# Kernel optimization log

Hardware: AMD Instinct MI355X
Metric: run time of the kernel (lower is better)

The kernel has to match this reference:

```python
import jax, jax.numpy as jnp
import numpy as np

EMBED_DIM = 768
NUM_HEADS = 12
NUM_BOND_TYPES = 4
NEG_INF = -1e9


def setup_inputs() -> dict:
    key = jax.random.key(0)
    ks = jax.random.split(key, 8)
    B, N, E = 32, 512, EMBED_DIM
    x = jax.random.normal(ks[0], (B, N, E), dtype=jnp.float32)
    adj = jax.random.randint(ks[1], (B, N, N), 0, 2, dtype=jnp.int32)
    bond = jax.random.randint(ks[2], (B, N, N), 0, NUM_BOND_TYPES + 1, dtype=jnp.int32)
    # nn.Linear(E, 3E): weight (3E, E), bias (3E)
    lim_qkv = 1.0 / np.sqrt(E)
    qkv_w = jax.random.uniform(ks[3], (3 * E, E), minval=-lim_qkv, maxval=lim_qkv, dtype=jnp.float32)
    qkv_b = jax.random.uniform(ks[4], (3 * E,), minval=-lim_qkv, maxval=lim_qkv, dtype=jnp.float32)
    out_w = jax.random.uniform(ks[5], (E, E), minval=-lim_qkv, maxval=lim_qkv, dtype=jnp.float32)
    out_b = jax.random.uniform(ks[6], (E,), minval=-lim_qkv, maxval=lim_qkv, dtype=jnp.float32)
    # nn.Embedding(num_bond_types+1, 1), padding_idx=0 -> row 0 is zero
    bond_table = jax.random.normal(ks[7], (NUM_BOND_TYPES + 1, 1), dtype=jnp.float32)
    bond_table = bond_table.at[0].set(0.0)
    return {"x": x, "adj": adj, "bond": bond, "num_heads": NUM_HEADS,
            "qkv_w": qkv_w, "qkv_b": qkv_b, "out_w": out_w, "out_b": out_b,
            "bond_table": bond_table}


def reference(x, adj, bond, num_heads, qkv_w, qkv_b, out_w, out_b, bond_table):
    B, N, E = x.shape
    hd = E // num_heads
    scale = hd ** -0.5
    # enforce padding_idx=0 semantics
    bond_table = bond_table.at[0].set(0.0)
    qkv = x @ qkv_w.T + qkv_b                      # (B, N, 3E)
    qkv = qkv.reshape(B, N, 3, num_heads, hd).transpose(2, 0, 3, 1, 4)
    q, k, v = qkv[0], qkv[1], qkv[2]               # (B, h, N, hd)
    attn = jnp.einsum('bhnd,bhmd->bhnm', q, k) * scale
    attn = attn + adj.astype(x.dtype)[:, None, :, :]
    bond_bias = bond_table[bond, 0]                # (B, N, N) embedding gather
    attn = attn + bond_bias[:, None, :, :]
    attn = jnp.where(attn == 0, NEG_INF, attn)     # masked_fill(attn == 0)
    attn = jax.nn.softmax(attn, axis=-1)
    out = jnp.einsum('bhnm,bhmd->bhnd', attn, v)   # (B, h, N, hd)
    out = out.transpose(0, 2, 1, 3).reshape(B, N, E)
    return out @ out_w.T + out_b
```

## Files before the change

kernel.cpp:

```cpp
#include <hip/hip_runtime.h>
#include <hip/hip_bf16.h>

typedef __attribute__((ext_vector_type(8))) short short8;
typedef __attribute__((ext_vector_type(4))) float f32x4;
typedef __attribute__((ext_vector_type(4))) unsigned int uint4v;
typedef __attribute__((ext_vector_type(4))) int int4v;

#define MFMA16(a,b,c) __builtin_amdgcn_mfma_f32_16x16x32_bf16((a),(b),(c),0,0,0)

#define GLOAD_LDS16(g, l) \
    __builtin_amdgcn_global_load_lds((const __attribute__((address_space(1))) void*)(g), \
                                     (__attribute__((address_space(3))) void*)(l), 16, 0, 0)

__device__ __forceinline__ unsigned short f2bf(float f){
    union { float f; unsigned int u; } c; c.f = f;
    unsigned int u = c.u;
    u = (u + 0x7fffu + ((u >> 16) & 1u)) >> 16;
    return (unsigned short)u;
}
__device__ __forceinline__ float bf2f(unsigned short s){
    union { unsigned int u; float f; } c; c.u = ((unsigned int)s) << 16;
    return c.f;
}

__device__ __forceinline__ void tsplit(float f, unsigned short &h, unsigned short &l){
    unsigned int u = __builtin_bit_cast(unsigned int, f);
    float hi = __builtin_bit_cast(float, u & 0xffff0000u);
    h = (unsigned short)(u >> 16);
    l = (unsigned short)(__builtin_bit_cast(unsigned int, f - hi) >> 16);
}

__device__ __forceinline__ unsigned int pack_split(float f){
    unsigned int u = __builtin_bit_cast(unsigned int, f);
    float hi = __builtin_bit_cast(float, u & 0xffff0000u);
    unsigned int rem = __builtin_bit_cast(unsigned int, f - hi);
    return __builtin_amdgcn_perm(rem, u, 0x07060302u);
}

__device__ __forceinline__ void unpack8(uint4v u0, uint4v u1, short8& hi, short8& lo){
    uint4v h, l;
    h[0] = __builtin_amdgcn_perm(u0[1], u0[0], 0x05040100u);
    h[1] = __builtin_amdgcn_perm(u0[3], u0[2], 0x05040100u);
    h[2] = __builtin_amdgcn_perm(u1[1], u1[0], 0x05040100u);
    h[3] = __builtin_amdgcn_perm(u1[3], u1[2], 0x05040100u);
    l[0] = __builtin_amdgcn_perm(u0[1], u0[0], 0x07060302u);
    l[1] = __builtin_amdgcn_perm(u0[3], u0[2], 0x07060302u);
    l[2] = __builtin_amdgcn_perm(u1[1], u1[0], 0x07060302u);
    l[3] = __builtin_amdgcn_perm(u1[3], u1[2], 0x07060302u);
    hi = __builtin_bit_cast(short8, h);
    lo = __builtin_bit_cast(short8, l);
}


__global__ void pack_x_kernel(const float* __restrict__ x, unsigned int* __restrict__ img){
    int tid = blockIdx.x * 256 + threadIdx.x;
    int m = tid / 96, grp = tid - m * 96;
    const float* src = x + (size_t)m * 768 + grp * 8;
    f32x4 v0 = ((const f32x4*)src)[0];
    f32x4 v1 = ((const f32x4*)src)[1];
    short8 h8, l8;
    #pragma unroll
    for (int j = 0; j < 4; ++j){
        unsigned short hh, ll;
        tsplit(v0[j], hh, ll); h8[j]   = (short)hh; l8[j]   = (short)ll;
        tsplit(v1[j], hh, ll); h8[4+j] = (short)hh; l8[4+j] = (short)ll;
    }
    int mt = m >> 7, row = m & 127, kt = grp >> 2, gi = grp & 3;
    int sw = (row & 7) << 4;
    char* bp = (char*)img + ((size_t)(mt*24 + kt))*16384 + row*128;
    *(short8*)(bp + ((gi*32     ) ^ sw)) = h8;
    *(short8*)(bp + ((gi*32 + 16) ^ sw)) = l8;
}

__global__ void pack_w_kernel(const float* __restrict__ wsrc, unsigned int* __restrict__ img, int total){
    int tid = blockIdx.x * 256 + threadIdx.x;
    if (tid >= total) return;
    int n = tid / 96, grp = tid - n * 96;
    const float* src = wsrc + (size_t)n * 768 + grp * 8;
    f32x4 v0 = ((const f32x4*)src)[0];
    f32x4 v1 = ((const f32x4*)src)[1];
    short8 h8, l8;
    #pragma unroll
    for (int j = 0; j < 4; ++j){
        unsigned short hh = f2bf(v0[j]);
        h8[j] = (short)hh; l8[j] = (short)f2bf(v0[j] - bf2f(hh));
        hh = f2bf(v1[j]);
        h8[4+j] = (short)hh; l8[4+j] = (short)f2bf(v1[j] - bf2f(hh));
    }
    int jt = n >> 7, row = n & 127, kt = grp >> 2, gi = grp & 3;
    int sw = (row & 7) << 4;
    char* bp = (char*)img + ((size_t)(jt*24 + kt))*16384 + row*128;
    *(short8*)(bp + ((gi*32     ) ^ sw)) = h8;
    *(short8*)(bp + ((gi*32 + 16) ^ sw)) = l8;
}

__global__ void bias_kernel(const int* __restrict__ adj, const int* __restrict__ bond,
                            const float* __restrict__ table, float* __restrict__ biasC, int n4){
    int i = blockIdx.x * 256 + threadIdx.x;
    if (i >= n4) return;
    int4v a  = ((const int4v*)adj)[i];
    int4v bd = ((const int4v*)bond)[i];
    const float t1 = table[1], t2 = table[2], t3 = table[3], t4 = table[4];
    f32x4 o;
    #pragma unroll
    for (int j = 0; j < 4; ++j){
        int bv = bd[j];
        float tb = (bv == 1) ? t1 : (bv == 2) ? t2 : (bv == 3) ? t3 : (bv == 4) ? t4 : 0.0f;
        o[j] = (float)a[j] + tb;
    }
    ((f32x4*)biasC)[i] = o;
}

template<int EMODE>
__global__ __launch_bounds__(256, 3)
void gemm_img(const unsigned int* __restrict__ Aimg, const unsigned int* __restrict__ Bimg,
              const float* __restrict__ bias, int NT, int RPX,
              float* __restrict__ C, int N,
              char* __restrict__ qo, char* __restrict__ ko, char* __restrict__ vo)
{
    __shared__ unsigned int lds[8192];

    const int lin = blockIdx.x;
    const int xcd = lin & 7, idx = lin >> 3;
    const int grp  = idx / (RPX * 6);
    const int rem  = idx - grp * (RPX * 6);
    const int rowL = rem / 6, c6 = rem - rowL * 6;
    const int colT = grp * 6 + c6;
    const int mt = xcd * RPX + rowL;
    const int m0 = mt << 7, j0 = colT << 7;

    const int t = threadIdx.x, l = t & 63, w = t >> 6;
    const int c = l & 15, g = l >> 4;
    const int wr = (w >> 1) * 64, wc2 = (w & 1) * 64;

    const unsigned int* Ablk = Aimg + (size_t)mt   * NT * 4096;
    const unsigned int* Bblk = Bimg + (size_t)colT * NT * 4096;

    f32x4 acc[4][4] = {};

    for (int kt = 0; kt < NT; ++kt){
        const unsigned int* As = Ablk + kt*4096 + t*4;
        const unsigned int* Bs = Bblk + kt*4096 + t*4;
        unsigned int* Ad = lds + t*4;
        unsigned int* Bd = lds + 4096 + t*4;
        #pragma unroll
        for (int i = 0; i < 4; ++i){
            GLOAD_LDS16(As + i*1024, Ad + i*1024);
            GLOAD_LDS16(Bs + i*1024, Bd + i*1024);
        }
        __syncthreads();

        short8 bh[4], bl[4];
        #pragma unroll
        for (int fc = 0; fc < 4; ++fc){
            int row = wc2 + fc*16 + c;
            int sw = (row & 7) << 4;
            const char* p = (const char*)(lds + 4096) + row*128;
            bh[fc] = *(const short8*)(p + ((g*32     ) ^ sw));
            bl[fc] = *(const short8*)(p + ((g*32 + 16) ^ sw));
        }
        #pragma unroll
        for (int fr = 0; fr < 4; ++fr){
            int row = wr + fr*16 + c;
            int sw = (row & 7) << 4;
            const char* p = (const char*)lds + row*128;
            short8 ah = *(const short8*)(p + ((g*32     ) ^ sw));
            short8 al = *(const short8*)(p + ((g*32 + 16) ^ sw));
            __builtin_amdgcn_s_setprio(1);
            #pragma unroll
            for (int fc = 0; fc < 4; ++fc){
                acc[fr][fc] = MFMA16(ah, bh[fc], acc[fr][fc]);
                acc[fr][fc] = MFMA16(ah, bl[fc], acc[fr][fc]);
                acc[fr][fc] = MFMA16(al, bh[fc], acc[fr][fc]);
            }
            __builtin_amdgcn_s_setprio(0);
        }
        __syncthreads();
    }

    #pragma unroll
    for (int fr = 0; fr < 4; ++fr){
        #pragma unroll
        for (int fc = 0; fc < 4; ++fc){
            #pragma unroll
            for (int r = 0; r < 4; ++r){
                int m = m0 + wr + fr*16 + g*4 + r;
                int j = j0 + wc2 + fc*16 + c;
                float val = acc[fr][fc][r] + bias[j];
                if constexpr (EMODE == 0){
                    C[(size_t)m * N + j] = val;
                } else {
                    int sec = j / 768;
                    int off = j - sec * 768;
                    int head = off >> 6, d = off & 63;
                    int bb = m >> 9, n = m & 511;
                    int bh2 = bb * 12 + head;
                    unsigned short hh, ll;
                    tsplit(val, hh, ll);
                    if (sec == 0) {
                        char* p = qo + ((size_t)bh2*512 + n)*256 + (d>>3)*32 + (d&7)*2;
                        *(unsigned short*)(p     ) = hh;
                        *(unsigned short*)(p + 16) = ll;
                    } else if (sec == 1) {
                        int row = n & 63, sw = (row & 7) << 4;
                        char* p = ko + (size_t)(bh2*8 + (n>>6))*16384 + row*256;
                        *(unsigned short*)(p + ((((d>>3)*32)     ) ^ sw) + (d&7)*2) = hh;
                        *(unsigned short*)(p + ((((d>>3)*32) + 16) ^ sw) + (d&7)*2) = ll;
                    } else {
                        int col = n & 63, sw = (d & 7) << 4;
                        char* p = vo + (size_t)(bh2*8 + (n>>6))*16384 + d*256;
                        *(unsigned short*)(p + ((((col>>3)*32)     ) ^ sw) + (col&7)*2) = hh;
                        *(unsigned short*)(p + ((((col>>3)*32) + 16) ^ sw) + (col&7)*2) = ll;
                    }
                }
            }
        }
    }
}

__global__ __launch_bounds__(256, 3)
void attn_kernel(const char* __restrict__ qb,
                 const unsigned int* __restrict__ kimg,
                 const unsigned int* __restrict__ vimg,
                 const float* __restrict__ biasC,
                 char* __restrict__ oimg)
{
    __shared__ unsigned int Kt[4096];
    __shared__ unsigned int Vt[4096];
    __shared__ unsigned int Pt[4][16 * 68];

    const int lin = blockIdx.x;
    const int xcd = lin & 7, m_ = lin >> 3;
    const int bgrp = m_ / 96, r_ = m_ - bgrp * 96;
    const int b = (bgrp << 3) | xcd;
    const int h = r_ >> 3, qt = r_ & 7;
    const int bh = b * 12 + h, q0 = qt * 64;

    const int t = threadIdx.x, l = t & 63, w = t >> 6;
    const int c = l & 15, g = l >> 4;

    short8 qh[2], ql[2];
    {
        int qrow = q0 + w*16 + c;
        const char* qp = qb + ((size_t)bh*512 + qrow)*256;
        #pragma unroll
        for (int ks = 0; ks < 2; ++ks){
            qh[ks] = *(const short8*)(qp + ks*128 + g*32);
            ql[ks] = *(const short8*)(qp + ks*128 + g*32 + 16);
        }
    }

    f32x4 O[4] = {};
    float mrow[4] = {-3e38f, -3e38f, -3e38f, -3e38f};
    float lrow[4] = {0.f, 0.f, 0.f, 0.f};

    auto rdfrag = [&](const unsigned int* base, int row, int colb, short8& hi, short8& lo){
        int sw = (row & 7) << 4;
        const char* p = (const char*)base + row*256;
        hi = *(const short8*)(p + ((colb     ) ^ sw));
        lo = *(const short8*)(p + ((colb + 16) ^ sw));
    };

    for (int kt = 0; kt < 8; ++kt){
        {
            const unsigned int* kg = kimg + (size_t)(bh*8 + kt)*4096 + t*4;
            const unsigned int* vg = vimg + (size_t)(bh*8 + kt)*4096 + t*4;
            #pragma unroll
            for (int i = 0; i < 4; ++i){
                GLOAD_LDS16(kg + i*1024, &Kt[t*4 + i*1024]);
                GLOAD_LDS16(vg + i*1024, &Vt[t*4 + i*1024]);
            }
        }

        float bia[4][4];
        #pragma unroll
        for (int fc = 0; fc < 4; ++fc){
            #pragma unroll
            for (int r = 0; r < 4; ++r){
                int rr = q0 + w*16 + g*4 + r;
                int cc = kt*64 + fc*16 + c;
                bia[fc][r] = biasC[((size_t)b * 512 + rr) * 512 + cc];
            }
        }
        __syncthreads();

        f32x4 S[4] = {};
        #pragma unroll
        for (int fc = 0; fc < 4; ++fc){
            short8 kbh0, kbl0, kbh1, kbl1;
            rdfrag(Kt, fc*16 + c,       g*32, kbh0, kbl0);
            rdfrag(Kt, fc*16 + c, 128 + g*32, kbh1, kbl1);
            __builtin_amdgcn_s_setprio(1);
            S[fc] = MFMA16(qh[0], kbh0, S[fc]);
            S[fc] = MFMA16(qh[0], kbl0, S[fc]);
            S[fc] = MFMA16(ql[0], kbh0, S[fc]);
            S[fc] = MFMA16(qh[1], kbh1, S[fc]);
            S[fc] = MFMA16(qh[1], kbl1, S[fc]);
            S[fc] = MFMA16(ql[1], kbh1, S[fc]);
            __builtin_amdgcn_s_setprio(0);
        }

        float sv[4][4];
        #pragma unroll
        for (int fc = 0; fc < 4; ++fc){
            #pragma unroll
            for (int r = 0; r < 4; ++r){
                float val = fmaf(S[fc][r], 0.125f, bia[fc][r]);
                if (val == 0.0f) val = -1e9f;
                sv[fc][r] = val;
            }
        }

        float pvreg[4][4];
        #pragma unroll
        for (int r = 0; r < 4; ++r){
            float mt = fmaxf(fmaxf(sv[0][r], sv[1][r]), fmaxf(sv[2][r], sv[3][r]));
            #pragma unroll
            for (int off = 1; off < 16; off <<= 1)
                mt = fmaxf(mt, __shfl_xor(mt, off, 16));
            float mn = fmaxf(mrow[r], mt);
            float corr = __expf(mrow[r] - mn);
            float rs = 0.0f;
            #pragma unroll
            for (int fc = 0; fc < 4; ++fc){
                float p = __expf(sv[fc][r] - mn);
                pvreg[fc][r] = p;
                rs += p;
            }
            #pragma unroll
            for (int off = 1; off < 16; off <<= 1)
                rs += __shfl_xor(rs, off, 16);
            lrow[r] = lrow[r] * corr + rs;
            mrow[r] = mn;
            #pragma unroll
            for (int hf = 0; hf < 4; ++hf)
                O[hf][r] *= corr;
        }

        #pragma unroll
        for (int fc = 0; fc < 4; ++fc){
            #pragma unroll
            for (int r = 0; r < 4; ++r){
                Pt[w][(g*4 + r)*68 + fc*16 + c] = pack_split(pvreg[fc][r]);
            }
        }

        #pragma unroll
        for (int ks = 0; ks < 2; ++ks){
            const unsigned int* pp = &Pt[w][c*68 + ks*32 + g*8];
            uint4v pu0 = *(const uint4v*)pp;
            uint4v pu1 = *(const uint4v*)(pp + 4);
            short8 pah, pal;
            unpack8(pu0, pu1, pah, pal);
            #pragma unroll
            for (int hf = 0; hf < 4; ++hf){
                short8 vbh, vbl;
                rdfrag(Vt, hf*16 + c, ks*128 + g*32, vbh, vbl);
                __builtin_amdgcn_s_setprio(1);
                O[hf] = MFMA16(pah, vbh, O[hf]);
                O[hf] = MFMA16(pah, vbl, O[hf]);
                O[hf] = MFMA16(pal, vbh, O[hf]);
                __builtin_amdgcn_s_setprio(0);
            }
        }
        __syncthreads();
    }

    #pragma unroll
    for (int r = 0; r < 4; ++r){
        float inv = 1.0f / lrow[r];
        int m = b*512 + q0 + w*16 + g*4 + r;
        int mt = m >> 7, mrow2 = m & 127;
        int swz = (mrow2 & 7) << 4;
        char* rowp = oimg + ((size_t)mt*24)*16384 + (size_t)mrow2*128;
        #pragma unroll
        for (int hf = 0; hf < 4; ++hf){
            int e = h*64 + hf*16 + c;
            int kt2 = e >> 5, gi = (e >> 3) & 3, pos = e & 7;
            unsigned short hh, ll;
            tsplit(O[hf][r] * inv, hh, ll);
            char* p = rowp + (size_t)kt2*16384;
            *(unsigned short*)(p + (((gi*32)     ) ^ swz) + pos*2) = hh;
            *(unsigned short*)(p + (((gi*32) + 16) ^ swz) + pos*2) = ll;
        }
    }
}

extern "C" void kernel_launch(void* const* d_in, const int* in_sizes, int n_in,
                              void* d_out, int out_size, void* d_ws, size_t ws_size,
                              hipStream_t stream)
{
    const float* x     = (const float*)d_in[0];
    const int*   adj   = (const int*)d_in[1];
    const int*   bond  = (const int*)d_in[2];
    const float* qkv_w = (const float*)d_in[4];
    const float* qkv_b = (const float*)d_in[5];
    const float* out_w = (const float*)d_in[6];
    const float* out_b = (const float*)d_in[7];
    const float* btab  = (const float*)d_in[8];
    float* out = (float*)d_out;

    const size_t QKV = 12582912;
    unsigned int* q   = (unsigned int*)d_ws;
    unsigned int* k   = q  + QKV;
    unsigned int* vt  = k  + QKV;
    unsigned int* r1  = vt + QKV;
    unsigned int* w2i = r1 + QKV;
    unsigned int* r2  = w2i + 589824;
    unsigned int* w1i = r2;
    float* biasC      = (float*)r2;

    dim3 blk(256);
    pack_w_kernel<<<dim3(864), blk, 0, stream>>>(qkv_w, w1i, 2304*96);
    pack_w_kernel<<<dim3(288), blk, 0, stream>>>(out_w, w2i, 768*96);
    pack_x_kernel<<<dim3(6144), blk, 0, stream>>>(x, r1);

    gemm_img<1><<<dim3(2304), blk, 0, stream>>>(r1, w1i, qkv_b, 24, 16,
                                                nullptr, 2304, (char*)q, (char*)k, (char*)vt);

    bias_kernel<<<dim3(8192), blk, 0, stream>>>(adj, bond, btab, biasC, (32*512*512)/4);

    attn_kernel<<<dim3(3072), blk, 0, stream>>>((const char*)q, k, vt, biasC, (char*)r1);

    gemm_img<0><<<dim3(768), blk, 0, stream>>>(r1, w2i, out_b, 24, 16,
                                               out, 768, nullptr, nullptr, nullptr);
}
```

Before: 415.4 us.

## Compute transposed S tile so P stays in registers, dropping LDS round-trip

```diff
diff --git a/kernel.cpp b/kernel.cpp
--- a/kernel.cpp
+++ b/kernel.cpp
@@ -28,27 +28,6 @@
     float hi = __builtin_bit_cast(float, u & 0xffff0000u);
     h = (unsigned short)(u >> 16);
     l = (unsigned short)(__builtin_bit_cast(unsigned int, f - hi) >> 16);
-}
-
-__device__ __forceinline__ unsigned int pack_split(float f){
-    unsigned int u = __builtin_bit_cast(unsigned int, f);
-    float hi = __builtin_bit_cast(float, u & 0xffff0000u);
-    unsigned int rem = __builtin_bit_cast(unsigned int, f - hi);
-    return __builtin_amdgcn_perm(rem, u, 0x07060302u);
-}
-
-__device__ __forceinline__ void unpack8(uint4v u0, uint4v u1, short8& hi, short8& lo){
-    uint4v h, l;
-    h[0] = __builtin_amdgcn_perm(u0[1], u0[0], 0x05040100u);
-    h[1] = __builtin_amdgcn_perm(u0[3], u0[2], 0x05040100u);
-    h[2] = __builtin_amdgcn_perm(u1[1], u1[0], 0x05040100u);
-    h[3] = __builtin_amdgcn_perm(u1[3], u1[2], 0x05040100u);
-    l[0] = __builtin_amdgcn_perm(u0[1], u0[0], 0x07060302u);
-    l[1] = __builtin_amdgcn_perm(u0[3], u0[2], 0x07060302u);
-    l[2] = __builtin_amdgcn_perm(u1[1], u1[0], 0x07060302u);
-    l[3] = __builtin_amdgcn_perm(u1[3], u1[2], 0x07060302u);
-    hi = __builtin_bit_cast(short8, h);
-    lo = __builtin_bit_cast(short8, l);
 }
 
 
@@ -202,10 +181,11 @@
                         *(unsigned short*)(p     ) = hh;
                         *(unsigned short*)(p + 16) = ll;
                     } else if (sec == 1) {
-                        int row = n & 63, sw = (row & 7) << 4;
+                        int row = n & 63;
+                        int ksw = (((row & 7) + (((row >> 3) & 3) << 1)) & 7) << 4;
                         char* p = ko + (size_t)(bh2*8 + (n>>6))*16384 + row*256;
-                        *(unsigned short*)(p + ((((d>>3)*32)     ) ^ sw) + (d&7)*2) = hh;
-                        *(unsigned short*)(p + ((((d>>3)*32) + 16) ^ sw) + (d&7)*2) = ll;
+                        *(unsigned short*)(p + ((((d>>3)*32)     ) ^ ksw) + (d&7)*2) = hh;
+                        *(unsigned short*)(p + ((((d>>3)*32) + 16) ^ ksw) + (d&7)*2) = ll;
                     } else {
                         int col = n & 63, sw = (d & 7) << 4;
                         char* p = vo + (size_t)(bh2*8 + (n>>6))*16384 + d*256;
@@ -218,7 +198,7 @@
     }
 }
 
-__global__ __launch_bounds__(256, 3)
+__global__ __launch_bounds__(256, 4)
 void attn_kernel(const char* __restrict__ qb,
                  const unsigned int* __restrict__ kimg,
                  const unsigned int* __restrict__ vimg,
@@ -227,7 +207,6 @@
 {
     __shared__ unsigned int Kt[4096];
     __shared__ unsigned int Vt[4096];
-    __shared__ unsigned int Pt[4][16 * 68];
 
     const int lin = blockIdx.x;
     const int xcd = lin & 7, m_ = lin >> 3;
@@ -251,15 +230,9 @@
     }
 
     f32x4 O[4] = {};
-    float mrow[4] = {-3e38f, -3e38f, -3e38f, -3e38f};
-    float lrow[4] = {0.f, 0.f, 0.f, 0.f};
-
-    auto rdfrag = [&](const unsigned int* base, int row, int colb, short8& hi, short8& lo){
-        int sw = (row & 7) << 4;
-        const char* p = (const char*)base + row*256;
-        hi = *(const short8*)(p + ((colb     ) ^ sw));
-        lo = *(const short8*)(p + ((colb + 16) ^ sw));
-    };
+    float m_run = -3e38f, l_run = 0.0f;
+
+    const float* biasRow = biasC + ((size_t)b * 512 + (q0 + w*16 + c)) * 512;
 
     for (int kt = 0; kt < 8; ++kt){
         {
@@ -272,90 +245,96 @@
             }
         }
 
-        float bia[4][4];
-        #pragma unroll
-        for (int fc = 0; fc < 4; ++fc){
-            #pragma unroll
-            for (int r = 0; r < 4; ++r){
-                int rr = q0 + w*16 + g*4 + r;
-                int cc = kt*64 + fc*16 + c;
-                bia[fc][r] = biasC[((size_t)b * 512 + rr) * 512 + cc];
-            }
+        f32x4 bia[4];
+        #pragma unroll
+        for (int fc = 0; fc < 4; ++fc){
+            int keyb = kt*64 + (fc>>1)*32 + g*8 + ((fc&1)<<2);
+            bia[fc] = *(const f32x4*)(biasRow + keyb);
         }
         __syncthreads();
 
         f32x4 S[4] = {};
         #pragma unroll
         for (int fc = 0; fc < 4; ++fc){
-            short8 kbh0, kbl0, kbh1, kbl1;
-            rdfrag(Kt, fc*16 + c,       g*32, kbh0, kbl0);
-            rdfrag(Kt, fc*16 + c, 128 + g*32, kbh1, kbl1);
+            int row = (fc>>1)*32 + ((c>>2)<<3) + ((fc&1)<<2) + (c&3);
+            int ksw = (((row & 7) + (((row >> 3) & 3) << 1)) & 7) << 4;
+            const char* kp = (const char*)Kt + row*256;
+            short8 kbh0 = *(const short8*)(kp + ((g*32           ) ^ ksw));
+            short8 kbl0 = *(const short8*)(kp + ((g*32 + 16      ) ^ ksw));
+            short8 kbh1 = *(const short8*)(kp + ((128 + g*32     ) ^ ksw));
+            short8 kbl1 = *(const short8*)(kp + ((128 + g*32 + 16) ^ ksw));
             __builtin_amdgcn_s_setprio(1);
-            S[fc] = MFMA16(qh[0], kbh0, S[fc]);
-            S[fc] = MFMA16(qh[0], kbl0, S[fc]);
-            S[fc] = MFMA16(ql[0], kbh0, S[fc]);
-            S[fc] = MFMA16(qh[1], kbh1, S[fc]);
-            S[fc] = MFMA16(qh[1], kbl1, S[fc]);
-            S[fc] = MFMA16(ql[1], kbh1, S[fc]);
+            S[fc] = MFMA16(kbh0, qh[0], S[fc]);
+            S[fc] = MFMA16(kbl0, qh[0], S[fc]);
+            S[fc] = MFMA16(kbh0, ql[0], S[fc]);
+            S[fc] = MFMA16(kbh1, qh[1], S[fc]);
+            S[fc] = MFMA16(kbl1, qh[1], S[fc]);
+            S[fc] = MFMA16(kbh1, ql[1], S[fc]);
             __builtin_amdgcn_s_setprio(0);
         }
 
-        float sv[4][4];
+        float p[4][4];
+        float pmax = -3e38f;
         #pragma unroll
         for (int fc = 0; fc < 4; ++fc){
             #pragma unroll
             for (int r = 0; r < 4; ++r){
                 float val = fmaf(S[fc][r], 0.125f, bia[fc][r]);
                 if (val == 0.0f) val = -1e9f;
-                sv[fc][r] = val;
-            }
-        }
-
-        float pvreg[4][4];
+                p[fc][r] = val;
+                pmax = fmaxf(pmax, val);
+            }
+        }
+        pmax = fmaxf(pmax, __shfl_xor(pmax, 16));
+        pmax = fmaxf(pmax, __shfl_xor(pmax, 32));
+        float mn = fmaxf(m_run, pmax);
+        float corr = __expf(m_run - mn);
+        float rs = 0.0f;
+        #pragma unroll
+        for (int fc = 0; fc < 4; ++fc){
+            #pragma unroll
+            for (int r = 0; r < 4; ++r){
+                float e = __expf(p[fc][r] - mn);
+                p[fc][r] = e;
+                rs += e;
+            }
+        }
+        rs += __shfl_xor(rs, 16);
+        rs += __shfl_xor(rs, 32);
+        l_run = l_run * corr + rs;
+        m_run = mn;
+
         #pragma unroll
         for (int r = 0; r < 4; ++r){
-            float mt = fmaxf(fmaxf(sv[0][r], sv[1][r]), fmaxf(sv[2][r], sv[3][r]));
-            #pragma unroll
-            for (int off = 1; off < 16; off <<= 1)
-                mt = fmaxf(mt, __shfl_xor(mt, off, 16));
-            float mn = fmaxf(mrow[r], mt);
-            float corr = __expf(mrow[r] - mn);
-            float rs = 0.0f;
-            #pragma unroll
-            for (int fc = 0; fc < 4; ++fc){
-                float p = __expf(sv[fc][r] - mn);
-                pvreg[fc][r] = p;
-                rs += p;
-            }
-            #pragma unroll
-            for (int off = 1; off < 16; off <<= 1)
-                rs += __shfl_xor(rs, off, 16);
-            lrow[r] = lrow[r] * corr + rs;
-            mrow[r] = mn;
-            #pragma unroll
-            for (int hf = 0; hf < 4; ++hf)
-                O[hf][r] *= corr;
-        }
-
-        #pragma unroll
-        for (int fc = 0; fc < 4; ++fc){
-            #pragma unroll
-            for (int r = 0; r < 4; ++r){
-                Pt[w][(g*4 + r)*68 + fc*16 + c] = pack_split(pvreg[fc][r]);
-            }
+            float cr = __shfl(corr, (l & 48) | (g*4 + r));
+            O[0][r] *= cr; O[1][r] *= cr; O[2][r] *= cr; O[3][r] *= cr;
         }
 
         #pragma unroll
         for (int ks = 0; ks < 2; ++ks){
-            const unsigned int* pp = &Pt[w][c*68 + ks*32 + g*8];
-            uint4v pu0 = *(const uint4v*)pp;
-            uint4v pu1 = *(const uint4v*)(pp + 4);
-            short8 pah, pal;
-            unpack8(pu0, pu1, pah, pal);
+            uint4v ph, plo;
+            #pragma unroll
+            for (int j = 0; j < 4; ++j){
+                const int fc = 2*ks + (j >> 1);
+                const int r0 = (j & 1) * 2;
+                float a  = p[fc][r0], bq = p[fc][r0 + 1];
+                unsigned int ua = __builtin_bit_cast(unsigned int, a);
+                unsigned int ub = __builtin_bit_cast(unsigned int, bq);
+                float ra = a  - __builtin_bit_cast(float, ua & 0xffff0000u);
+                float rb = bq - __builtin_bit_cast(float, ub & 0xffff0000u);
+                ph[j]  = __builtin_amdgcn_perm(ub, ua, 0x07060302u);
+                plo[j] = __builtin_amdgcn_perm(__builtin_bit_cast(unsigned int, rb),
+                                               __builtin_bit_cast(unsigned int, ra), 0x07060302u);
+            }
+            short8 pah = __builtin_bit_cast(short8, ph);
+            short8 pal = __builtin_bit_cast(short8, plo);
             #pragma unroll
             for (int hf = 0; hf < 4; ++hf){
-                short8 vbh, vbl;
-                rdfrag(Vt, hf*16 + c, ks*128 + g*32, vbh, vbl);
+                int row = hf*16 + c;
+                int sw = (row & 7) << 4;
+                const char* vp = (const char*)Vt + row*256;
+                short8 vbh = *(const short8*)(vp + ((ks*128 + g*32     ) ^ sw));
+                short8 vbl = *(const short8*)(vp + ((ks*128 + g*32 + 16) ^ sw));
                 __builtin_amdgcn_s_setprio(1);
                 O[hf] = MFMA16(pah, vbh, O[hf]);
                 O[hf] = MFMA16(pah, vbl, O[hf]);
@@ -366,9 +345,10 @@
         __syncthreads();
     }
 
+    float linv = 1.0f / l_run;
     #pragma unroll
     for (int r = 0; r < 4; ++r){
-        float inv = 1.0f / lrow[r];
+        float inv = __shfl(linv, (l & 48) | (g*4 + r));
         int m = b*512 + q0 + w*16 + g*4 + r;
         int mt = m >> 7, mrow2 = m & 127;
         int swz = (mrow2 & 7) << 4;
@@ -379,9 +359,9 @@
             int kt2 = e >> 5, gi = (e >> 3) & 3, pos = e & 7;
             unsigned short hh, ll;
             tsplit(O[hf][r] * inv, hh, ll);
-            char* p = rowp + (size_t)kt2*16384;
-            *(unsigned short*)(p + (((gi*32)     ) ^ swz) + pos*2) = hh;
-            *(unsigned short*)(p + (((gi*32) + 16) ^ swz) + pos*2) = ll;
+            char* pp = rowp + (size_t)kt2*16384;
+            *(unsigned short*)(pp + (((gi*32)     ) ^ swz) + pos*2) = hh;
+            *(unsigned short*)(pp + (((gi*32) + 16) ^ swz) + pos*2) = ll;
         }
     }
 }
```

Measured after the change: 389.3 us. 6.3% less time.
